# Kernel tuning notes

Hardware: AMD Instinct MI355X
Metric: run time of the kernel (lower is better)

The kernel has to match this reference:

```python
import jax, jax.numpy as jnp
import numpy as np

B, S, E, H = 4, 8192, 1024, 16
D = E // H  # head_dim = 64


def setup_inputs() -> dict:
    key = jax.random.key(0)
    ks = jax.random.split(key, 6)
    x = jax.random.normal(ks[0], (B, S, E), dtype=jnp.float32)
    key_padding_mask = jax.random.randint(ks[1], (B, S), 0, 2).astype(jnp.bool_)
    scale = 1.0 / np.sqrt(E)
    Wq = jax.random.normal(ks[2], (E, E), dtype=jnp.float32) * scale
    Wk = jax.random.normal(ks[3], (E, E), dtype=jnp.float32) * scale
    Wv = jax.random.normal(ks[4], (E, E), dtype=jnp.float32) * scale
    Wo = jax.random.normal(ks[5], (E, E), dtype=jnp.float32) * scale
    return {"x": x, "key_padding_mask": key_padding_mask,
            "Wq": Wq, "Wk": Wk, "Wv": Wv, "Wo": Wo}


def reference(x, key_padding_mask, Wq, Wk, Wv, Wo):
    b, s, _ = x.shape
    # torch Linear (no bias): y = x @ W.T
    Q = (x @ Wq.T).reshape(b, s, H, D).transpose(0, 2, 1, 3)  # (b,h,s,d)
    K = (x @ Wk.T).reshape(b, s, H, D).transpose(0, 2, 1, 3)
    V = (x @ Wv.T).reshape(b, s, H, D).transpose(0, 2, 1, 3)
    Q = jax.nn.elu(Q) + 1.0
    K = jax.nn.elu(K) + 1.0
    mask = key_padding_mask[:, None, :, None]  # (b,1,s,1), True = padding
    K = jnp.where(mask, 0.0, K)
    V = jnp.where(mask, 0.0, V)
    # global KV summarization over sequence: (b,h,d,e)
    KV = jnp.einsum('bhsd,bhse->bhde', K, V)
    K_sum = K.sum(axis=2)  # (b,h,d)
    Z = 1.0 / (jnp.einsum('bhsd,bhd->bhs', Q, K_sum) + 1e-6)  # (b,h,s)
    out = jnp.einsum('bhsd,bhde->bhse', Q, KV) * Z[..., None]  # (b,h,s,e)
    out = out.transpose(0, 2, 1, 3).reshape(b, s, E)
    return out @ Wo.T
```

## Files before the change

kernel.cpp:

```cpp
#include <hip/hip_runtime.h>

#define NB 4
#define NS 8192
#define NE 1024
#define NH 16
#define ND 64
#define NM (NB*NS)

typedef __bf16 bf16x8 __attribute__((ext_vector_type(8)));
typedef float  f32x4  __attribute__((ext_vector_type(4)));

__device__ __forceinline__ unsigned short f2bf(float f){
  unsigned int u = __float_as_uint(f);
  u += 0x7FFFu + ((u >> 16) & 1u);
  return (unsigned short)(u >> 16);
}
__device__ __forceinline__ float bf2f(unsigned short h){
  return __uint_as_float(((unsigned int)h) << 16);
}
__device__ __forceinline__ void gload16(const void* g, void* lds){
  __builtin_amdgcn_global_load_lds(
      (__attribute__((address_space(1))) unsigned int*)g,
      (__attribute__((address_space(3))) unsigned int*)lds, 16, 0, 0);
}

__global__ void mask_prep(const void* mraw, unsigned char* mask_u8){
  __shared__ int flag_s;
  if (threadIdx.x == 0) flag_s = 0;
  __syncthreads();
  const unsigned int* mi = (const unsigned int*)mraw;
  int bad = 0;
  for (int i = threadIdx.x; i < 4096; i += 256) bad |= (mi[i] > 1u) ? 1 : 0;
  if (bad) atomicOr(&flag_s, 1);
  __syncthreads();
  const int isbyte = flag_s;
  const unsigned char* mb = (const unsigned char*)mraw;
  int stride = gridDim.x * blockDim.x;
  for (int i = blockIdx.x*blockDim.x + threadIdx.x; i < NM; i += stride)
    mask_u8[i] = isbyte ? (unsigned char)(mb[i] != 0) : (unsigned char)(mi[i] != 0);
}

struct CastJobs {
  const float* src[5];
  unsigned short* dst[5];
  int n4[5];
};

__global__ __launch_bounds__(256) void castk(CastJobs J){
  int j = blockIdx.y;
  const float* s = J.src[j];
  unsigned short* d = J.dst[j];
  int n4 = J.n4[j];
  int stride = gridDim.x * blockDim.x;
  for (int i = blockIdx.x*blockDim.x + threadIdx.x; i < n4; i += stride){
    float4 v = *(const float4*)(s + (long)i*4);
    ushort4 o;
    o.x = f2bf(v.x); o.y = f2bf(v.y); o.z = f2bf(v.z); o.w = f2bf(v.w);
    *(ushort4*)(d + (long)i*4) = o;
  }
}

__global__ __launch_bounds__(256) void gemm_bt(
    const unsigned short* __restrict__ A,
    const unsigned short* __restrict__ W0,
    const unsigned short* __restrict__ W1,
    const unsigned short* __restrict__ W2,
    unsigned short* __restrict__ O0,
    unsigned short* __restrict__ O1,
    unsigned short* __restrict__ O2,
    float* __restrict__ OF,
    const unsigned char* __restrict__ mask,
    int modeSel)
{
  __shared__ unsigned short As [128*32];
  __shared__ unsigned short Bsh[128*32];

  const int mode = (modeSel < 0) ? (int)blockIdx.y : modeSel;
  const unsigned short* Bw = (mode==0) ? W0 : (mode==1) ? W1 : (mode==2) ? W2 : W0;
  unsigned short* Obf = (mode==0) ? O0 : (mode==1) ? O1 : O2;

  const int nwg = (int)gridDim.x;
  const int bx  = (int)blockIdx.x;
  const int cpx = nwg >> 3;
  const int swz = (bx & 7) * cpx + (bx >> 3);
  const int mtile = swz >> 3;
  const int ntile = swz & 7;
  const long m0 = (long)mtile * 128;
  const int  n0 = ntile * 128;

  const int tid  = (int)threadIdx.x;
  const int lane = tid & 63;
  const int wv   = tid >> 6;
  const int l15  = lane & 15;
  const int hi   = lane >> 4;
  const int wrow = (wv >> 1) * 64;
  const int wcol = (wv & 1) * 64;

  const int rr = lane >> 2;
  const int kk = (lane & 3) * 8;

  f32x4 acc[4][4];
  #pragma unroll
  for (int i=0;i<4;++i)
    #pragma unroll
    for (int j=0;j<4;++j)
      acc[i][j] = (f32x4){0.f,0.f,0.f,0.f};

  for (int k0 = 0; k0 < NE; k0 += 32){
    if (k0) __syncthreads();
    #pragma unroll
    for (int j=0;j<2;++j){
      const int c = wv*2 + j;
      const int r = c*16 + rr;
      gload16(A  + (m0 + r)*NE + k0 + kk, &As [c*512]);
      gload16(Bw + (long)(n0 + r)*NE + k0 + kk, &Bsh[c*512]);
    }
    __syncthreads();
    bf16x8 av[4], bv[4];
    #pragma unroll
    for (int mi=0;mi<4;++mi)
      av[mi] = *(const bf16x8*)&As[(wrow + mi*16 + l15)*32 + hi*8];
    #pragma unroll
    for (int ni=0;ni<4;++ni)
      bv[ni] = *(const bf16x8*)&Bsh[(wcol + ni*16 + l15)*32 + hi*8];
    #pragma unroll
    for (int mi=0;mi<4;++mi)
      #pragma unroll
      for (int ni=0;ni<4;++ni)
        acc[mi][ni] = __builtin_amdgcn_mfma_f32_16x16x32_bf16(av[mi], bv[ni], acc[mi][ni], 0, 0, 0);
  }

  #pragma unroll
  for (int mi=0;mi<4;++mi){
    #pragma unroll
    for (int r=0;r<4;++r){
      const long mg = m0 + wrow + mi*16 + hi*4 + r;
      const bool mz = (mode==1 || mode==2) ? (mask[mg] != 0) : false;
      #pragma unroll
      for (int ni=0;ni<4;++ni){
        const int ng = n0 + wcol + ni*16 + l15;
        float v = acc[mi][ni][r];
        if (mode==0 || mode==1) v = (v > 0.f) ? (v + 1.f) : __expf(v);
        if (mz) v = 0.f;
        if (mode==3) OF[mg*NE + ng] = v;
        else         Obf[mg*NE + ng] = f2bf(v);
      }
    }
  }
}

#define KVCH 16
#define KVROWS (NS/KVCH)
__global__ __launch_bounds__(256) void kv_reduce(const unsigned short* __restrict__ K,
                                                 const unsigned short* __restrict__ V,
                                                 float* __restrict__ part){
  __shared__ float lds[2*64*68 + 192];
  float* Ksf = lds;
  float* Vsf = lds + 64*68;
  float* kcorner = lds + 2*64*68;

  const int bid = blockIdx.x;
  const int bh = bid >> 4;
  const int chunk = bid & 15;
  const int b = bh >> 4, h = bh & 15;
  const int t = threadIdx.x, w = t >> 6, l = t & 63;
  const int dg = l & 15, eg = l >> 4;
  const long base = ((long)b*NS + (long)chunk*KVROWS)*NE + h*ND;

  f32x4 acc[4][4];
  #pragma unroll
  for (int j=0;j<4;++j)
    #pragma unroll
    for (int q=0;q<4;++q)
      acc[j][q] = (f32x4){0.f,0.f,0.f,0.f};
  f32x4 ks4 = (f32x4){0.f,0.f,0.f,0.f};

  for (int sc = 0; sc < KVROWS/64; ++sc){
    if (sc) __syncthreads();
    const long rbase = base + (long)sc*64*NE;
    #pragma unroll
    for (int p = 0; p < 4; ++p){
      int g = p*256 + t;
      int row = g >> 4, col = (g & 15)*4;
      ushort4 ku = *(const ushort4*)(K + rbase + (long)row*NE + col);
      ushort4 vu = *(const ushort4*)(V + rbase + (long)row*NE + col);
      f32x4 kf = { bf2f(ku.x), bf2f(ku.y), bf2f(ku.z), bf2f(ku.w) };
      f32x4 vf = { bf2f(vu.x), bf2f(vu.y), bf2f(vu.z), bf2f(vu.w) };
      *(f32x4*)&Ksf[row*68 + col] = kf;
      *(f32x4*)&Vsf[row*68 + col] = vf;
    }
    __syncthreads();
    #pragma unroll 2
    for (int i = 0; i < 16; ++i){
      const int r = w*16 + i;
      f32x4 kq = *(const f32x4*)&Ksf[r*68 + dg*4];
      f32x4 v0 = *(const f32x4*)&Vsf[r*68 + eg*16 + 0];
      f32x4 v1 = *(const f32x4*)&Vsf[r*68 + eg*16 + 4];
      f32x4 v2 = *(const f32x4*)&Vsf[r*68 + eg*16 + 8];
      f32x4 v3 = *(const f32x4*)&Vsf[r*68 + eg*16 + 12];
      #pragma unroll
      for (int j=0;j<4;++j){
        const float kd = kq[j];
        acc[j][0] += kd * v0;
        acc[j][1] += kd * v1;
        acc[j][2] += kd * v2;
        acc[j][3] += kd * v3;
      }
      if (eg == 0) ks4 += kq;
    }
  }

  __syncthreads();
  if (w >= 1 && eg == 0)
    *(f32x4*)&kcorner[(w-1)*64 + dg*4] = ks4;
  if (w >= 2){
    float* reg = (w==2) ? Ksf : Vsf;
    #pragma unroll
    for (int j=0;j<4;++j)
      #pragma unroll
      for (int q=0;q<4;++q)
        *(f32x4*)&reg[l*68 + (j*4+q)*4] = acc[j][q];
  }
  __syncthreads();
  if (w < 2){
    float* reg = (w==0) ? Ksf : Vsf;
    #pragma unroll
    for (int j=0;j<4;++j)
      #pragma unroll
      for (int q=0;q<4;++q)
        acc[j][q] += *(const f32x4*)&reg[l*68 + (j*4+q)*4];
  }
  __syncthreads();
  if (w == 1){
    #pragma unroll
    for (int j=0;j<4;++j)
      #pragma unroll
      for (int q=0;q<4;++q)
        *(f32x4*)&Ksf[l*68 + (j*4+q)*4] = acc[j][q];
  }
  __syncthreads();
  if (w == 0){
    #pragma unroll
    for (int j=0;j<4;++j)
      #pragma unroll
      for (int q=0;q<4;++q)
        acc[j][q] += *(const f32x4*)&Ksf[l*68 + (j*4+q)*4];
    float* po = part + (long)(bh*16 + chunk)*4160;
    #pragma unroll
    for (int j=0;j<4;++j)
      #pragma unroll
      for (int q=0;q<4;++q)
        *(f32x4*)&po[(dg*4 + j)*64 + eg*16 + q*4] = acc[j][q];
    if (eg == 0){
      #pragma unroll
      for (int i=0;i<3;++i)
        ks4 += *(const f32x4*)&kcorner[i*64 + dg*4];
      *(f32x4*)&po[4096 + dg*4] = ks4;
    }
  }
}

__global__ __launch_bounds__(256) void kv_finish(const float* __restrict__ part,
                                                 unsigned short* __restrict__ KVfrag){
  __shared__ float KVf[64*65 + 32];
  const int bh = blockIdx.x, t = threadIdx.x;
  const float* pb = part + (long)bh*16*4160;

  #pragma unroll
  for (int p = 0; p < 4; ++p){
    int g = p*256 + t;
    f32x4 s = (f32x4){0.f,0.f,0.f,0.f};
    for (int c = 0; c < 16; ++c) s += *(const f32x4*)&pb[c*4160 + g*4];
    int d = g >> 4, e = (g & 15)*4;
    KVf[d*65 + e+0] = s[0];
    KVf[d*65 + e+1] = s[1];
    KVf[d*65 + e+2] = s[2];
    KVf[d*65 + e+3] = s[3];
  }
  if (t < 16){
    f32x4 s = (f32x4){0.f,0.f,0.f,0.f};
    for (int c = 0; c < 16; ++c) s += *(const f32x4*)&pb[c*4160 + 4096 + t*4];
    #pragma unroll
    for (int j=0;j<4;++j) KVf[(t*4+j)*65 + 64] = s[j];
  }
  __syncthreads();

  for (int idx = t; idx < 10240; idx += 256){
    int j   = idx & 7;
    int lfr = (idx >> 3) & 63;
    int grp = idx >> 9;
    int nt  = grp % 5, ks = grp / 5;
    int kk  = (ks & 1)*32 + (lfr >> 4)*8 + j;
    int n   = nt*16 + (lfr & 15);
    float v = (n <= 64) ? KVf[kk*65 + n] : 0.f;
    unsigned short hi = f2bf(v);
    unsigned short o  = (ks >> 1) ? f2bf(v - bf2f(hi)) : hi;
    KVfrag[(long)bh*10240 + idx] = o;
  }
}

__global__ __launch_bounds__(256) void attn_mfma(const unsigned short* __restrict__ Q,
                                                 const unsigned short* __restrict__ KVfrag,
                                                 unsigned short* __restrict__ attn){
  __shared__ unsigned short Qs[256*64];
  const int bid = blockIdx.x;
  const int bh = bid >> 5, chunk = bid & 31;
  const int b = bh >> 4, h = bh & 15;
  const int t = threadIdx.x, w = t >> 6, l = t & 63;
  const int l15 = l & 15, lhi = l >> 4;
  const long row0 = (long)b*NS + chunk*256;

  const int srccol = ((l & 7) ^ (l >> 3)) * 8;
  #pragma unroll
  for (int c = 0; c < 8; ++c){
    const int r = w*64 + c*8 + (l >> 3);
    gload16(Q + (row0 + r)*NE + h*ND + srccol, &Qs[(w*8 + c)*512]);
  }

  bf16x8 bf[4][5];
  #pragma unroll
  for (int ks=0; ks<4; ++ks)
    #pragma unroll
    for (int nt=0; nt<5; ++nt)
      bf[ks][nt] = *(const bf16x8*)(KVfrag + (long)bh*10240 + (ks*5+nt)*512 + l*8);

  __syncthreads();

  const int swz = (l15 & 7) << 4;
  const char* qbase = (const char*)&Qs[w*4096];

  #pragma unroll
  for (int rt=0; rt<4; ++rt){
    const int rb = (rt*16 + l15)*128;
    bf16x8 a0 = *(const bf16x8*)(qbase + rb + ((lhi*16) ^ swz));
    bf16x8 a1 = *(const bf16x8*)(qbase + rb + ((64 + lhi*16) ^ swz));
    f32x4 acc[5];
    #pragma unroll
    for (int nt=0; nt<5; ++nt){
      acc[nt] = (f32x4){0.f,0.f,0.f,0.f};
      acc[nt] = __builtin_amdgcn_mfma_f32_16x16x32_bf16(a0, bf[0][nt], acc[nt], 0,0,0);
      acc[nt] = __builtin_amdgcn_mfma_f32_16x16x32_bf16(a1, bf[1][nt], acc[nt], 0,0,0);
      acc[nt] = __builtin_amdgcn_mfma_f32_16x16x32_bf16(a0, bf[2][nt], acc[nt], 0,0,0);
      acc[nt] = __builtin_amdgcn_mfma_f32_16x16x32_bf16(a1, bf[3][nt], acc[nt], 0,0,0);
    }
    float dv[4];
    #pragma unroll
    for (int e=0;e<4;++e){
      float d = __shfl(acc[4][e], l & 48, 64);
      dv[e] = 1.f / (d + 1e-6f);
    }
    #pragma unroll
    for (int nt=0; nt<4; ++nt){
      #pragma unroll
      for (int e=0;e<4;++e){
        const int row = rt*16 + lhi*4 + e;
        const int cb  = (nt*16 + l15)*2;
        Qs[w*4096 + ((row*128 + (cb ^ ((row & 7) << 4))) >> 1)] = f2bf(acc[nt][e] * dv[e]);
      }
    }
  }

  asm volatile("s_waitcnt lgkmcnt(0)" ::: "memory");
  #pragma unroll
  for (int c=0;c<8;++c){
    const int r = c*8 + (l >> 3);
    bf16x8 vv = *(const bf16x8*)((const char*)&Qs[w*4096] + r*128 + ((((l&7) ^ (l>>3))) << 4));
    *(bf16x8*)(attn + (row0 + w*64 + r)*NE + h*ND + (l&7)*8) = vv;
  }
}

extern "C" void kernel_launch(void* const* d_in, const int* in_sizes, int n_in,
                              void* d_out, int out_size, void* d_ws, size_t ws_size,
                              hipStream_t stream){
  (void)in_sizes; (void)n_in; (void)out_size; (void)ws_size;
  const float* x    = (const float*)d_in[0];
  const void*  mraw = d_in[1];
  const float* Wq   = (const float*)d_in[2];
  const float* Wk   = (const float*)d_in[3];
  const float* Wv   = (const float*)d_in[4];
  const float* Wo   = (const float*)d_in[5];
  float* out = (float*)d_out;
  char* ws = (char*)d_ws;

  unsigned short* xb  = (unsigned short*)(ws + 0L);
  unsigned short* Wqb = (unsigned short*)(ws + 67108864L);
  unsigned short* Wkb = (unsigned short*)(ws + 69206016L);
  unsigned short* Wvb = (unsigned short*)(ws + 71303168L);
  unsigned short* Wob = (unsigned short*)(ws + 73400320L);
  unsigned short* Qb  = (unsigned short*)(ws + 75497472L);
  unsigned short* Kb  = (unsigned short*)(ws + 142606336L);
  unsigned short* Vb  = (unsigned short*)(ws + 209715200L);
  unsigned short* KVfrag = (unsigned short*)(ws + 276824064L);
  unsigned char* mask_u8 = (unsigned char*)(ws + 278462464L);
  float* part = (float*)xb;

  mask_prep<<<32, 256, 0, stream>>>(mraw, mask_u8);

  CastJobs J;
  J.src[0]=x;  J.dst[0]=xb;  J.n4[0]=NM*NE/4;
  J.src[1]=Wq; J.dst[1]=Wqb; J.n4[1]=NE*NE/4;
  J.src[2]=Wk; J.dst[2]=Wkb; J.n4[2]=NE*NE/4;
  J.src[3]=Wv; J.dst[3]=Wvb; J.n4[3]=NE*NE/4;
  J.src[4]=Wo; J.dst[4]=Wob; J.n4[4]=NE*NE/4;
  castk<<<dim3(1024,5), 256, 0, stream>>>(J);

  gemm_bt<<<dim3(2048,3), 256, 0, stream>>>(xb, Wqb, Wkb, Wvb,
                                            Qb, Kb, Vb, nullptr, mask_u8, -1);

  kv_reduce<<<dim3(1024), 256, 0, stream>>>(Kb, Vb, part);
  kv_finish<<<dim3(64), 256, 0, stream>>>(part, KVfrag);

  attn_mfma<<<dim3(2048), 256, 0, stream>>>(Qb, KVfrag, xb);

  gemm_bt<<<dim3(2048,1), 256, 0, stream>>>(xb, Wob, Wob, Wob,
                                            nullptr, nullptr, nullptr, out, mask_u8, 3);
}
```

Before: 512.1 us.

## Replace 128x128 GEMM with double-buffered 256x256 tile kernel using 8 waves

Replaces the simple 128x128, K=32 single-buffered projection GEMM with a 256x256 tile, K=64 kernel run by 512 threads (8 waves). It double-buffers the LDS staging with async global-to-LDS loads, uses an XOR-swizzled LDS layout to avoid bank conflicts, and interleaves quarter-stage loads with MFMA clusters using setprio and explicit waitcnt. The aim is more reuse per byte loaded and hiding memory latency behind compute in the four projection GEMMs. In exchange it uses 128 KB of LDS per block and more registers, and correctness depends on delicate hand-tuned vmcnt and barrier counts.

```diff
diff --git a/kernel.cpp b/kernel.cpp
--- a/kernel.cpp
+++ b/kernel.cpp
@@ -6,6 +6,7 @@
 #define NH 16
 #define ND 64
 #define NM (NB*NS)
+#define NKT 16
 
 typedef __bf16 bf16x8 __attribute__((ext_vector_type(8)));
 typedef float  f32x4  __attribute__((ext_vector_type(4)));
@@ -60,7 +61,7 @@
   }
 }
 
-__global__ __launch_bounds__(256) void gemm_bt(
+__global__ __launch_bounds__(512, 2) void gemm256(
     const unsigned short* __restrict__ A,
     const unsigned short* __restrict__ W0,
     const unsigned short* __restrict__ W1,
@@ -72,8 +73,8 @@
     const unsigned char* __restrict__ mask,
     int modeSel)
 {
-  __shared__ unsigned short As [128*32];
-  __shared__ unsigned short Bsh[128*32];
+  __shared__ __align__(16) unsigned short As[2*256*64];
+  __shared__ __align__(16) unsigned short Bs[2*256*64];
 
   const int mode = (modeSel < 0) ? (int)blockIdx.y : modeSel;
   const unsigned short* Bw = (mode==0) ? W0 : (mode==1) ? W1 : (mode==2) ? W2 : W0;
@@ -81,64 +82,154 @@
 
   const int nwg = (int)gridDim.x;
   const int bx  = (int)blockIdx.x;
-  const int cpx = nwg >> 3;
-  const int swz = (bx & 7) * cpx + (bx >> 3);
-  const int mtile = swz >> 3;
-  const int ntile = swz & 7;
-  const long m0 = (long)mtile * 128;
-  const int  n0 = ntile * 128;
-
-  const int tid  = (int)threadIdx.x;
-  const int lane = tid & 63;
-  const int wv   = tid >> 6;
-  const int l15  = lane & 15;
-  const int hi   = lane >> 4;
-  const int wrow = (wv >> 1) * 64;
-  const int wcol = (wv & 1) * 64;
-
-  const int rr = lane >> 2;
-  const int kk = (lane & 3) * 8;
-
-  f32x4 acc[4][4];
-  #pragma unroll
-  for (int i=0;i<4;++i)
+  const int swz = (bx & 7) * (nwg >> 3) + (bx >> 3);
+  const long m0 = (long)(swz >> 2) * 256;
+  const int  n0 = (swz & 3) * 256;
+
+  const int tid = (int)threadIdx.x;
+  const int l   = tid & 63;
+  const int wv  = tid >> 6;
+  const int wr  = wv >> 2;
+  const int wc  = wv & 3;
+  const int l15 = l & 15;
+  const int lhi = l >> 4;
+  const int swz8 = (l & 7) * 8;
+
+  const int srow = wv*16 + (l >> 3);
+  const int scol = ((l & 7) * 8) ^ ((l >> 3) << 3);
+
+  auto stageA = [&](int st, int h){
+    const long col = (long)st*64 + scol;
+    #pragma unroll
+    for (int is = 0; is < 2; ++is)
+      gload16(A + (m0 + h*128 + srow + is*8)*NE + col,
+              &As[(st & 1)*16384 + h*8192 + (wv*2 + is)*512]);
+  };
+  auto stageB = [&](int st, int h){
+    const long col = (long)st*64 + scol;
+    #pragma unroll
+    for (int is = 0; is < 2; ++is)
+      gload16(Bw + (long)(n0 + h*128 + srow + is*8)*NE + col,
+              &Bs[(st & 1)*16384 + h*8192 + (wv*2 + is)*512]);
+  };
+  auto stageQ = [&](int s){
+    if (s >= 4*NKT) return;
+    const int st = s >> 2, qq = s & 3;
+    if (qq & 2) stageB(st, qq & 1); else stageA(st, qq & 1);
+  };
+
+  auto lda = [&](int buf, int mi, int ks)->bf16x8 {
+    const int row = wr*128 + mi*16 + l15;
+    const int col = (ks*32 + lhi*8) ^ swz8;
+    return *(const bf16x8*)&As[buf*16384 + row*64 + col];
+  };
+  auto ldb = [&](int buf, int ni, int ks)->bf16x8 {
+    const int row = wc*64 + ni*16 + l15;
+    const int col = (ks*32 + lhi*8) ^ swz8;
+    return *(const bf16x8*)&Bs[buf*16384 + row*64 + col];
+  };
+
+  f32x4 acc[8][4];
+  #pragma unroll
+  for (int i=0;i<8;++i)
     #pragma unroll
     for (int j=0;j<4;++j)
       acc[i][j] = (f32x4){0.f,0.f,0.f,0.f};
 
-  for (int k0 = 0; k0 < NE; k0 += 32){
-    if (k0) __syncthreads();
-    #pragma unroll
-    for (int j=0;j<2;++j){
-      const int c = wv*2 + j;
-      const int r = c*16 + rr;
-      gload16(A  + (m0 + r)*NE + k0 + kk, &As [c*512]);
-      gload16(Bw + (long)(n0 + r)*NE + k0 + kk, &Bsh[c*512]);
-    }
-    __syncthreads();
-    bf16x8 av[4], bv[4];
-    #pragma unroll
-    for (int mi=0;mi<4;++mi)
-      av[mi] = *(const bf16x8*)&As[(wrow + mi*16 + l15)*32 + hi*8];
-    #pragma unroll
-    for (int ni=0;ni<4;++ni)
-      bv[ni] = *(const bf16x8*)&Bsh[(wcol + ni*16 + l15)*32 + hi*8];
-    #pragma unroll
-    for (int mi=0;mi<4;++mi)
-      #pragma unroll
-      for (int ni=0;ni<4;++ni)
-        acc[mi][ni] = __builtin_amdgcn_mfma_f32_16x16x32_bf16(av[mi], bv[ni], acc[mi][ni], 0, 0, 0);
-  }
-
-  #pragma unroll
-  for (int mi=0;mi<4;++mi){
+  stageQ(0); stageQ(1); stageQ(2); stageQ(3);
+  asm volatile("s_waitcnt vmcnt(4)" ::: "memory");
+  stageQ(4); stageQ(5); stageQ(6);
+  asm volatile("s_waitcnt vmcnt(6)" ::: "memory");
+  __builtin_amdgcn_s_barrier();
+
+  bf16x8 a0[4][2], a1[4][2], b0[2][2], b1[2][2];
+
+  #pragma unroll 2
+  for (int kt = 0; kt < NKT; ++kt){
+    const int buf = kt & 1;
+    const int sb  = 7 + 4*kt;
+
+    #pragma unroll
+    for (int i=0;i<4;++i){ a0[i][0]=lda(buf,i,0); a0[i][1]=lda(buf,i,1); }
+    #pragma unroll
+    for (int j=0;j<2;++j){ b0[j][0]=ldb(buf,j,0); b0[j][1]=ldb(buf,j,1); }
+    stageQ(sb+0);
+    asm volatile("s_waitcnt lgkmcnt(8)" ::: "memory");
+    __builtin_amdgcn_s_barrier();
+    asm volatile("s_waitcnt lgkmcnt(0)" ::: "memory");
+    __builtin_amdgcn_sched_barrier(0);
+    __builtin_amdgcn_s_setprio(1);
+    #pragma unroll
+    for (int ks=0;ks<2;++ks)
+      #pragma unroll
+      for (int i=0;i<4;++i)
+        #pragma unroll
+        for (int j=0;j<2;++j)
+          acc[i][j] = __builtin_amdgcn_mfma_f32_16x16x32_bf16(a0[i][ks], b0[j][ks], acc[i][j], 0,0,0);
+    __builtin_amdgcn_s_setprio(0);
+    __builtin_amdgcn_s_barrier();
+
+    #pragma unroll
+    for (int i=0;i<4;++i){ a1[i][0]=lda(buf,4+i,0); a1[i][1]=lda(buf,4+i,1); }
+    stageQ(sb+1);
+    __builtin_amdgcn_s_barrier();
+    asm volatile("s_waitcnt lgkmcnt(0)" ::: "memory");
+    __builtin_amdgcn_sched_barrier(0);
+    __builtin_amdgcn_s_setprio(1);
+    #pragma unroll
+    for (int ks=0;ks<2;++ks)
+      #pragma unroll
+      for (int i=0;i<4;++i)
+        #pragma unroll
+        for (int j=0;j<2;++j)
+          acc[4+i][j] = __builtin_amdgcn_mfma_f32_16x16x32_bf16(a1[i][ks], b0[j][ks], acc[4+i][j], 0,0,0);
+    __builtin_amdgcn_s_setprio(0);
+    __builtin_amdgcn_s_barrier();
+
+    #pragma unroll
+    for (int j=0;j<2;++j){ b1[j][0]=ldb(buf,2+j,0); b1[j][1]=ldb(buf,2+j,1); }
+    stageQ(sb+2);
+    __builtin_amdgcn_s_barrier();
+    asm volatile("s_waitcnt lgkmcnt(0)" ::: "memory");
+    __builtin_amdgcn_sched_barrier(0);
+    __builtin_amdgcn_s_setprio(1);
+    #pragma unroll
+    for (int ks=0;ks<2;++ks)
+      #pragma unroll
+      for (int i=0;i<4;++i)
+        #pragma unroll
+        for (int j=0;j<2;++j)
+          acc[4+i][2+j] = __builtin_amdgcn_mfma_f32_16x16x32_bf16(a1[i][ks], b1[j][ks], acc[4+i][2+j], 0,0,0);
+    __builtin_amdgcn_s_setprio(0);
+    __builtin_amdgcn_s_barrier();
+
+    stageQ(sb+3);
+    __builtin_amdgcn_s_barrier();
+    asm volatile("s_waitcnt lgkmcnt(0)" ::: "memory");
+    __builtin_amdgcn_sched_barrier(0);
+    __builtin_amdgcn_s_setprio(1);
+    #pragma unroll
+    for (int ks=0;ks<2;++ks)
+      #pragma unroll
+      for (int i=0;i<4;++i)
+        #pragma unroll
+        for (int j=0;j<2;++j)
+          acc[i][2+j] = __builtin_amdgcn_mfma_f32_16x16x32_bf16(a0[i][ks], b1[j][ks], acc[i][2+j], 0,0,0);
+    __builtin_amdgcn_s_setprio(0);
+    if (kt < NKT-2)       asm volatile("s_waitcnt vmcnt(6)" ::: "memory");
+    else if (kt == NKT-2) asm volatile("s_waitcnt vmcnt(0)" ::: "memory");
+    __builtin_amdgcn_s_barrier();
+  }
+
+  #pragma unroll
+  for (int mi=0;mi<8;++mi){
     #pragma unroll
     for (int r=0;r<4;++r){
-      const long mg = m0 + wrow + mi*16 + hi*4 + r;
+      const long mg = m0 + wr*128 + mi*16 + lhi*4 + r;
       const bool mz = (mode==1 || mode==2) ? (mask[mg] != 0) : false;
       #pragma unroll
       for (int ni=0;ni<4;++ni){
-        const int ng = n0 + wcol + ni*16 + l15;
+        const int ng = n0 + wc*64 + ni*16 + l15;
         float v = acc[mi][ni][r];
         if (mode==0 || mode==1) v = (v > 0.f) ? (v + 1.f) : __expf(v);
         if (mz) v = 0.f;
@@ -404,14 +495,14 @@
   J.src[4]=Wo; J.dst[4]=Wob; J.n4[4]=NE*NE/4;
   castk<<<dim3(1024,5), 256, 0, stream>>>(J);
 
-  gemm_bt<<<dim3(2048,3), 256, 0, stream>>>(xb, Wqb, Wkb, Wvb,
-                                            Qb, Kb, Vb, nullptr, mask_u8, -1);
+  gemm256<<<dim3(512,3), 512, 0, stream>>>(xb, Wqb, Wkb, Wvb,
+                                           Qb, Kb, Vb, nullptr, mask_u8, -1);
 
   kv_reduce<<<dim3(1024), 256, 0, stream>>>(Kb, Vb, part);
   kv_finish<<<dim3(64), 256, 0, stream>>>(part, KVfrag);
 
   attn_mfma<<<dim3(2048), 256, 0, stream>>>(Qb, KVfrag, xb);
 
-  gemm_bt<<<dim3(2048,1), 256, 0, stream>>>(xb, Wob, Wob, Wob,
-                                            nullptr, nullptr, nullptr, out, mask_u8, 3);
-}
+  gemm256<<<dim3(512,1), 512, 0, stream>>>(xb, Wob, Wob, Wob,
+                                           nullptr, nullptr, nullptr, out, mask_u8, 3);
+}
```

Result: faster. 476.8 us (-6.9%).
